# Optimization experiments

Measured on AMD Instinct MI355X. Metric: run time of the kernel, lower is better.

## Reference

```python
import jax, jax.numpy as jnp
import numpy as np

B, M, SV, OV, R, L, V, E = 256, 10, 32, 32, 128, 12, 1000, 64
M2 = M * M
STATE_DIM = (SV + 1) * M2  # 3300
OBJ_DIM = OV * M2          # 3200


def setup_inputs() -> dict:
    key = jax.random.key(0)
    ks = jax.random.split(key, 24)
    s = 0.02
    inp = {
        "state": jax.random.randint(ks[0], (B, M2), 0, SV),
        "obj": jax.random.randint(ks[1], (B, M2), 0, OV),
        "text": jax.random.randint(ks[2], (B, L), 0, V),
        # state MLP [STATE_DIM,128,128,R]
        "Ws1": jax.random.normal(ks[3], (STATE_DIM, 128)) * s,
        "bs1": jnp.zeros((128,)),
        "Ws2": jax.random.normal(ks[4], (128, 128)) * s,
        "bs2": jnp.zeros((128,)),
        "Ws3": jax.random.normal(ks[5], (128, R)) * s,
        "bs3": jnp.zeros((R,)),
        # object MLP [OBJ_DIM,128,128,R]
        "Wo1": jax.random.normal(ks[6], (OBJ_DIM, 128)) * s,
        "bo1": jnp.zeros((128,)),
        "Wo2": jax.random.normal(ks[7], (128, 128)) * s,
        "bo2": jnp.zeros((128,)),
        "Wo3": jax.random.normal(ks[8], (128, R)) * s,
        "bo3": jnp.zeros((R,)),
        # LSTM text encoder: embedding + single-layer LSTM with hidden=R
        "emb": jax.random.normal(ks[9], (V, E)) * s,
        "Wih": jax.random.normal(ks[10], (E, 4 * R)) * s,
        "Whh": jax.random.normal(ks[11], (R, 4 * R)) * s,
        "b_lstm": jnp.zeros((4 * R,)),
    }
    return inp


def _mlp(x, W1, b1, W2, b2, W3, b3):
    h = jax.nn.relu(x @ W1 + b1)
    h = jax.nn.relu(h @ W2 + b2)
    return h @ W3 + b3


def _lstm_last_hidden(text, emb, Wih, Whh, b):
    # text: (B, L) ids -> final hidden (B, R)
    x = emb[text]                      # (B, L, E)
    xs = jnp.swapaxes(x, 0, 1)         # (L, B, E)
    h0 = jnp.zeros((text.shape[0], R), x.dtype)
    c0 = jnp.zeros((text.shape[0], R), x.dtype)

    def step(carry, xt):
        h, c = carry
        g = xt @ Wih + h @ Whh + b     # (B, 4R)
        i, f, gg, o = jnp.split(g, 4, axis=-1)
        c = jax.nn.sigmoid(f) * c + jax.nn.sigmoid(i) * jnp.tanh(gg)
        h = jax.nn.sigmoid(o) * jnp.tanh(c)
        return (h, c), None

    (h, _), _ = jax.lax.scan(step, (h0, c0), xs)
    return h


def reference(state, obj, text, Ws1, bs1, Ws2, bs2, Ws3, bs3,
              Wo1, bo1, Wo2, bo2, Wo3, bo3, emb, Wih, Whh, b_lstm):
    b = state.shape[0]
    # one-hot encodings (torch scatter_ over channel dim)
    state_oh = jax.nn.one_hot(state, SV, dtype=jnp.float32)   # (B, 100, SV)
    obj_oh = jax.nn.one_hot(obj, OV, dtype=jnp.float32)       # (B, 100, OV)

    # repeat each map map_dim^2 times; copy p gets a one-hot of agent position p
    pos = jnp.eye(M2, dtype=jnp.float32)[None, :, :, None]    # (1, 100 copies, 100 cells, 1)
    state_rep = jnp.broadcast_to(state_oh[:, None], (b, M2, M2, SV))
    state_inp = jnp.concatenate(
        [state_rep, jnp.broadcast_to(pos, (b, M2, M2, 1))], axis=-1
    ).reshape(b * M2, STATE_DIM)
    obj_inp = jnp.broadcast_to(obj_oh[:, None], (b, M2, M2, OV)).reshape(b * M2, OBJ_DIM)

    state_out = _mlp(state_inp, Ws1, bs1, Ws2, bs2, Ws3, bs3)   # (B*100, R)
    object_out = _mlp(obj_inp, Wo1, bo1, Wo2, bo2, Wo3, bo3)    # (B*100, R)

    # text is identical across the 100 copies -> encode once, broadcast
    h = _lstm_last_hidden(text, emb, Wih, Whh, b_lstm)          # (B, R)
    lstm_out = jnp.broadcast_to(h[:, None], (b, M2, R)).reshape(b * M2, R)

    values = state_out * object_out * lstm_out                 # (B*100, R)
    map_pred = values.sum(1).reshape(b, M, M)
    return map_pred
```

## Files before the change

kernel.cpp:

```cpp
#include <hip/hip_runtime.h>


#define B_   256
#define M2_  100
#define R_   128
#define L_   12
#define E_   64
#define NT   1024

typedef _Float16 half2v __attribute__((ext_vector_type(2)));
typedef _Float16 f16x8  __attribute__((ext_vector_type(8)));
typedef float    f32x4  __attribute__((ext_vector_type(4)));

__device__ __forceinline__ float sigf(float x) { return 1.f / (1.f + expf(-x)); }

__device__ __forceinline__ uint pk16(float a, float b) {
    half2v h; h.x = (_Float16)a; h.y = (_Float16)b;
    return __builtin_bit_cast(uint, h);
}

__global__ __launch_bounds__(256) void pack_kernel(
    const float* __restrict__ Whh, const float* __restrict__ Wih,
    const float* __restrict__ Ws2, void* __restrict__ wsv)
{
    _Float16* WhhT = (_Float16*)wsv;
    _Float16* WihT = WhhT + 65536;
    uint*     W2P  = (uint*)(WihT + 32768);
    int g = blockIdx.x * 256 + threadIdx.x;
    if (g < 65536) {
        int r = g >> 9, c = g & 511;
        WhhT[c * 128 + r] = (_Float16)Whh[r * 512 + c];
    } else if (g < 65536 + 32768) {
        int g2 = g - 65536;
        int e = g2 >> 9, c = g2 & 511;
        WihT[c * 64 + e] = (_Float16)Wih[e * 512 + c];
    } else if (g < 65536 + 32768 + 8192) {
        int g3 = g - 65536 - 32768;
        int jp = g3 >> 7, kk = g3 & 127;
        W2P[g3] = pk16(Ws2[(2 * jp) * R_ + kk], Ws2[(2 * jp + 1) * R_ + kk]);
    }
}

__global__ __launch_bounds__(NT) __attribute__((amdgpu_waves_per_eu(4, 4)))
void uvfa_kernel(
    const int* __restrict__ state, const int* __restrict__ obj, const int* __restrict__ text,
    const float* __restrict__ Ws1, const float* __restrict__ bs1,
    const float* __restrict__ bs2, const float* __restrict__ Ws3, const float* __restrict__ bs3,
    const float* __restrict__ Wo1, const float* __restrict__ bo1,
    const float* __restrict__ Wo2, const float* __restrict__ bo2,
    const float* __restrict__ Wo3, const float* __restrict__ bo3,
    const float* __restrict__ emb, const float* __restrict__ b_lstm,
    const _Float16* __restrict__ WhhT, const _Float16* __restrict__ WihT,
    const uint* __restrict__ W2P,
    float* __restrict__ out)
{
    const int b   = blockIdx.x;
    const int tid = threadIdx.x;

    __shared__ __align__(16) uint  U[16064];
    __shared__ __align__(16) float part[NT];
    __shared__ __align__(16) float hbuf[R_];
    __shared__ __align__(16) uint  hpair[R_ / 2];
    __shared__ __align__(16) float tmp[R_], tmp2[R_], wbuf[R_], ubuf[R_], bsbuf[R_];
    __shared__ float redw2[2][112];
    __shared__ int   idx_o[M2_], idx_s[M2_], tids[L_];
    __shared__ float c0s;

    float* xw   = (float*)U;
    float* xemb = (float*)(U + 8192);

    const int lane = tid & 63;
    const int wv   = tid >> 6;
    const int m16  = lane & 15;
    const int kgrp = lane >> 4;

    f16x8 af[2][4];
    #pragma unroll
    for (int tt = 0; tt < 2; ++tt) {
        int col = (2 * wv + tt) * 16 + m16;
        #pragma unroll
        for (int s = 0; s < 4; ++s)
            af[tt][s] = *(const f16x8*)&WhhT[col * 128 + s * 32 + kgrp * 8];
    }

    if (tid < M2_) idx_o[tid] = obj[b * M2_ + tid];
    else if (tid >= 128 && tid < 128 + M2_) idx_s[tid - 128] = state[b * M2_ + tid - 128];
    else if (tid >= 256 && tid < 256 + L_) tids[tid - 256] = text[b * L_ + tid - 256];
    else if (tid >= 384 && tid < 448) hpair[tid - 384] = 0u;
    __syncthreads();
    if (tid < L_ * E_) xemb[(tid >> 6) * 66 + (tid & 63)] = emb[tids[tid >> 6] * E_ + (tid & 63)];
    else if (tid < L_ * E_ + 264) ((float*)(U + 8192 + 792))[tid - L_ * E_] = 0.f;
    __syncthreads();

    {
        f16x8 ax[2];
        #pragma unroll
        for (int s = 0; s < 2; ++s) {
            #pragma unroll
            for (int e = 0; e < 8; ++e)
                ax[s][e] = (_Float16)xemb[m16 * 66 + s * 32 + kgrp * 8 + e];
        }
        #pragma unroll
        for (int h = 0; h < 2; ++h) {
            int col = (wv * 2 + h) * 16 + m16;
            float bl = b_lstm[col];
            f32x4 acc = { bl, bl, bl, bl };
            #pragma unroll
            for (int s = 0; s < 2; ++s) {
                f16x8 bx = *(const f16x8*)&WihT[col * 64 + s * 32 + kgrp * 8];
                acc = __builtin_amdgcn_mfma_f32_16x16x32_f16(ax[s], bx, acc, 0, 0, 0);
            }
            if (kgrp < 3) {
                #pragma unroll
                for (int r = 0; r < 4; ++r)
                    xw[(kgrp * 4 + r) * 512 + col] = acc[r];
            }
        }
    }
    __syncthreads();

    float cst = 0.f;
    for (int t = 0; t < L_; ++t) {
        f16x8 bf[4];
        #pragma unroll
        for (int s = 0; s < 4; ++s) {
            uint4 hb = *(const uint4*)&hpair[s * 16 + kgrp * 4];
            bf[s] = __builtin_bit_cast(f16x8, hb);
        }
        #pragma unroll
        for (int tt = 0; tt < 2; ++tt) {
            int colb = (2 * wv + tt) * 16 + kgrp * 4;
            f32x4 acc = *(const f32x4*)&xw[t * 512 + colb];
            #pragma unroll
            for (int s = 0; s < 4; ++s)
                acc = __builtin_amdgcn_mfma_f32_16x16x32_f16(af[tt][s], bf[s], acc, 0, 0, 0);
            if (m16 == 0) {
                part[colb + 0] = acc[0];
                part[colb + 1] = acc[1];
                part[colb + 2] = acc[2];
                part[colb + 3] = acc[3];
            }
        }
        __syncthreads();
        if (tid < R_) {
            float gi = part[tid], gf = part[R_ + tid], gg = part[2 * R_ + tid], go = part[3 * R_ + tid];
            cst = sigf(gf) * cst + sigf(gi) * tanhf(gg);
            float hn = sigf(go) * tanhf(cst);
            hbuf[tid] = hn;
            float hs = __shfl_down(hn, 1, 64);
            if (!(tid & 1)) hpair[tid >> 1] = pk16(hn, hs);
        }
        __syncthreads();
    }

    {
        const uint4* src = (const uint4*)W2P;
        #pragma unroll
        for (int idx = tid; idx < 2048; idx += NT) {
            uint4 v = src[idx];
            int jp = idx >> 5, kq = idx & 31;
            *(uint4*)&U[jp * 132 + kq * 4] = v;
        }
    }

    const int k = tid & 127, qq = tid >> 7;
    {
        float acc = 0.f;
        int c0i = qq * 13, c1i = c0i + 13 < M2_ ? c0i + 13 : M2_;
        for (int c = c0i; c < c1i; ++c)
            acc += Wo1[(c * 32 + idx_o[c]) * R_ + k];
        part[qq * R_ + k] = acc;
    }
    __syncthreads();
    if (tid < R_) {
        float a = bo1[tid];
        #pragma unroll
        for (int q8 = 0; q8 < 8; ++q8) a += part[q8 * R_ + tid];
        tmp[tid] = fmaxf(a, 0.f);
    }
    __syncthreads();
    {
        float s0 = 0.f, s1 = 0.f, s2 = 0.f, s3 = 0.f;
        int j0 = qq * 16;
        #pragma unroll
        for (int j = 0; j < 16; j += 4) {
            s0 = fmaf(tmp[j0 + j + 0], Wo2[(j0 + j + 0) * R_ + k], s0);
            s1 = fmaf(tmp[j0 + j + 1], Wo2[(j0 + j + 1) * R_ + k], s1);
            s2 = fmaf(tmp[j0 + j + 2], Wo2[(j0 + j + 2) * R_ + k], s2);
            s3 = fmaf(tmp[j0 + j + 3], Wo2[(j0 + j + 3) * R_ + k], s3);
        }
        part[qq * R_ + k] = (s0 + s1) + (s2 + s3);
    }
    __syncthreads();
    if (tid < R_) {
        float a = bo2[tid];
        #pragma unroll
        for (int q8 = 0; q8 < 8; ++q8) a += part[q8 * R_ + tid];
        tmp2[tid] = fmaxf(a, 0.f);
    }
    __syncthreads();
    {
        float s0 = 0.f, s1 = 0.f, s2 = 0.f, s3 = 0.f;
        int j0 = qq * 16;
        #pragma unroll
        for (int j = 0; j < 16; j += 4) {
            s0 = fmaf(tmp2[j0 + j + 0], Wo3[(j0 + j + 0) * R_ + k], s0);
            s1 = fmaf(tmp2[j0 + j + 1], Wo3[(j0 + j + 1) * R_ + k], s1);
            s2 = fmaf(tmp2[j0 + j + 2], Wo3[(j0 + j + 2) * R_ + k], s2);
            s3 = fmaf(tmp2[j0 + j + 3], Wo3[(j0 + j + 3) * R_ + k], s3);
        }
        part[qq * R_ + k] = (s0 + s1) + (s2 + s3);
    }
    __syncthreads();
    if (tid < R_) {
        float a = bo3[tid];
        #pragma unroll
        for (int q8 = 0; q8 < 8; ++q8) a += part[q8 * R_ + tid];
        wbuf[tid] = a * hbuf[tid];
    }
    __syncthreads();

    {
        float s0 = 0.f, s1 = 0.f, s2 = 0.f, s3 = 0.f;
        int j0 = qq * 16;
        const float4* w3 = reinterpret_cast<const float4*>(&Ws3[k * R_ + j0]);
        #pragma unroll
        for (int jj = 0; jj < 4; ++jj) {
            float4 v = w3[jj];
            s0 = fmaf(v.x, wbuf[j0 + jj * 4 + 0], s0);
            s1 = fmaf(v.y, wbuf[j0 + jj * 4 + 1], s1);
            s2 = fmaf(v.z, wbuf[j0 + jj * 4 + 2], s2);
            s3 = fmaf(v.w, wbuf[j0 + jj * 4 + 3], s3);
        }
        part[qq * R_ + k] = (s0 + s1) + (s2 + s3);
    }
    if (tid >= 960) {
        int j = tid - 960;
        float s = bs3[j] * wbuf[j] + bs3[j + 64] * wbuf[j + 64];
        s += __shfl_down(s, 32, 64);
        s += __shfl_down(s, 16, 64);
        s += __shfl_down(s, 8, 64);
        s += __shfl_down(s, 4, 64);
        s += __shfl_down(s, 2, 64);
        s += __shfl_down(s, 1, 64);
        if (j == 0) c0s = s;
    }
    __syncthreads();
    if (tid < R_) {
        float a = 0.f;
        #pragma unroll
        for (int q8 = 0; q8 < 8; ++q8) a += part[q8 * R_ + tid];
        ubuf[tid] = a;
    }
    __syncthreads();

    {
        float acc = 0.f;
        int c0i = qq * 13, c1i = c0i + 13 < M2_ ? c0i + 13 : M2_;
        for (int c = c0i; c < c1i; ++c)
            acc += Ws1[(c * 33 + idx_s[c]) * R_ + k];
        part[qq * R_ + k] = acc;
    }
    __syncthreads();
    if (tid < R_) {
        float a = bs1[tid];
        #pragma unroll
        for (int q8 = 0; q8 < 8; ++q8) a += part[q8 * R_ + tid];
        bsbuf[tid] = a;
    }
    __syncthreads();

    #pragma unroll 4
    for (int pass = 0; pass < 13; ++pass) {
        int idx = pass * NT + tid;
        if (idx < M2_ * R_) {
            int j = idx & 127, p = idx >> 7;
            float v = fmaxf(bsbuf[j] + Ws1[(p * 33 + 32) * R_ + j], 0.f);
            float v2 = __shfl_down(v, 1, 64);
            if (!(j & 1)) U[8448 + p * 68 + (j >> 1)] = pk16(v, v2);
        }
    }
    if (tid < 816) U[8448 + 6800 + tid] = 0u;
    __syncthreads();

    if (wv < 14) {
        const int mtile = wv >> 1, nhalf = wv & 1;
        const uint* Ap = U + 8448 + (mtile * 16 + m16) * 68;
        f16x8 A[4];
        #pragma unroll
        for (int s = 0; s < 4; ++s)
            A[s] = __builtin_bit_cast(f16x8, *(const uint4*)&Ap[s * 16 + kgrp * 4]);
        f32x4 acc[4] = { {0,0,0,0}, {0,0,0,0}, {0,0,0,0}, {0,0,0,0} };
        #pragma unroll
        for (int nt = 0; nt < 4; ++nt) {
            int ko = (nhalf * 4 + nt) * 16 + m16;
            #pragma unroll
            for (int s = 0; s < 4; ++s) {
                const uint* Bp = U + (s * 16 + kgrp * 4) * 132 + ko;
                uint4 bv = { Bp[0], Bp[132], Bp[264], Bp[396] };
                acc[nt] = __builtin_amdgcn_mfma_f32_16x16x32_f16(
                    A[s], __builtin_bit_cast(f16x8, bv), acc[nt], 0, 0, 0);
            }
        }
        float vs0 = 0.f, vs1 = 0.f, vs2 = 0.f, vs3 = 0.f;
        #pragma unroll
        for (int nt = 0; nt < 4; ++nt) {
            int ko = (nhalf * 4 + nt) * 16 + m16;
            float bb = bs2[ko], uu = ubuf[ko];
            vs0 = fmaf(fmaxf(acc[nt][0] + bb, 0.f), uu, vs0);
            vs1 = fmaf(fmaxf(acc[nt][1] + bb, 0.f), uu, vs1);
            vs2 = fmaf(fmaxf(acc[nt][2] + bb, 0.f), uu, vs2);
            vs3 = fmaf(fmaxf(acc[nt][3] + bb, 0.f), uu, vs3);
        }
        vs0 += __shfl_xor(vs0, 1, 64); vs0 += __shfl_xor(vs0, 2, 64);
        vs0 += __shfl_xor(vs0, 4, 64); vs0 += __shfl_xor(vs0, 8, 64);
        vs1 += __shfl_xor(vs1, 1, 64); vs1 += __shfl_xor(vs1, 2, 64);
        vs1 += __shfl_xor(vs1, 4, 64); vs1 += __shfl_xor(vs1, 8, 64);
        vs2 += __shfl_xor(vs2, 1, 64); vs2 += __shfl_xor(vs2, 2, 64);
        vs2 += __shfl_xor(vs2, 4, 64); vs2 += __shfl_xor(vs2, 8, 64);
        vs3 += __shfl_xor(vs3, 1, 64); vs3 += __shfl_xor(vs3, 2, 64);
        vs3 += __shfl_xor(vs3, 4, 64); vs3 += __shfl_xor(vs3, 8, 64);
        if (m16 == 0) {
            int pr = mtile * 16 + kgrp * 4;
            redw2[nhalf][pr + 0] = vs0;
            redw2[nhalf][pr + 1] = vs1;
            redw2[nhalf][pr + 2] = vs2;
            redw2[nhalf][pr + 3] = vs3;
        }
    }
    __syncthreads();

    if (tid < M2_)
        out[b * M2_ + tid] = c0s + redw2[0][tid] + redw2[1][tid];
}

extern "C" void kernel_launch(void* const* d_in, const int* in_sizes, int n_in,
                              void* d_out, int out_size, void* d_ws, size_t ws_size,
                              hipStream_t stream) {
    const int*   state  = (const int*)d_in[0];
    const int*   obj    = (const int*)d_in[1];
    const int*   text   = (const int*)d_in[2];
    const float* Ws1    = (const float*)d_in[3];
    const float* bs1    = (const float*)d_in[4];
    const float* Ws2    = (const float*)d_in[5];
    const float* bs2    = (const float*)d_in[6];
    const float* Ws3    = (const float*)d_in[7];
    const float* bs3    = (const float*)d_in[8];
    const float* Wo1    = (const float*)d_in[9];
    const float* bo1    = (const float*)d_in[10];
    const float* Wo2    = (const float*)d_in[11];
    const float* bo2    = (const float*)d_in[12];
    const float* Wo3    = (const float*)d_in[13];
    const float* bo3    = (const float*)d_in[14];
    const float* emb    = (const float*)d_in[15];
    const float* Wih    = (const float*)d_in[16];
    const float* Whh    = (const float*)d_in[17];
    const float* b_lstm = (const float*)d_in[18];
    float* out = (float*)d_out;

    _Float16* WhhT = (_Float16*)d_ws;
    _Float16* WihT = WhhT + 65536;
    uint*     W2P  = (uint*)(WihT + 32768);

    hipLaunchKernelGGL(pack_kernel, dim3(416), dim3(256), 0, stream, Whh, Wih, Ws2, d_ws);
    hipLaunchKernelGGL(uvfa_kernel, dim3(B_), dim3(NT), 0, stream,
                       state, obj, text, Ws1, bs1, bs2, Ws3, bs3,
                       Wo1, bo1, Wo2, bo2, Wo3, bo3, emb, b_lstm,
                       WhhT, WihT, W2P, out);
}
```

Before: 39.85 us.

## Split each batch across two 512-thread blocks with staggered phase ordering

The grid now has two blocks of 512 threads per batch element instead of one 1024-thread block. Each block recomputes the LSTM and the object and state first-layer work, then handles half of the 100 output positions in the final MFMA stage. The two blocks run the LSTM and MLP phases in opposite order, so their latency-bound serial sections can overlap on the device. The sigmoid and tanh now use fast __expf, and the Whh fragments are pinned in registers. In exchange, the shared preamble work is done twice, and the fast transcendentals lose some accuracy.

Result: slower. 46.52 us (+16.7%).

```diff
diff --git a/kernel.cpp b/kernel.cpp
--- a/kernel.cpp
+++ b/kernel.cpp
@@ -6,18 +6,21 @@
 #define R_   128
 #define L_   12
 #define E_   64
-#define NT   1024
+#define NT   512
 
 typedef _Float16 half2v __attribute__((ext_vector_type(2)));
 typedef _Float16 f16x8  __attribute__((ext_vector_type(8)));
 typedef float    f32x4  __attribute__((ext_vector_type(4)));
 
-__device__ __forceinline__ float sigf(float x) { return 1.f / (1.f + expf(-x)); }
+__device__ __forceinline__ float sigf(float x)   { return 1.f / (1.f + __expf(-x)); }
+__device__ __forceinline__ float tanhff(float x) { float e = __expf(-2.f * x); return (1.f - e) / (1.f + e); }
 
 __device__ __forceinline__ uint pk16(float a, float b) {
     half2v h; h.x = (_Float16)a; h.y = (_Float16)b;
     return __builtin_bit_cast(uint, h);
 }
+
+#define PINU4(v) asm volatile("" : "+v"(v.x), "+v"(v.y), "+v"(v.z), "+v"(v.w));
 
 __global__ __launch_bounds__(256) void pack_kernel(
     const float* __restrict__ Whh, const float* __restrict__ Wih,
@@ -29,14 +32,12 @@
     int g = blockIdx.x * 256 + threadIdx.x;
     if (g < 65536) {
         int r = g >> 9, c = g & 511;
-        WhhT[c * 128 + r] = (_Float16)Whh[r * 512 + c];
-    } else if (g < 65536 + 32768) {
-        int g2 = g - 65536;
-        int e = g2 >> 9, c = g2 & 511;
-        WihT[c * 64 + e] = (_Float16)Wih[e * 512 + c];
-    } else if (g < 65536 + 32768 + 8192) {
-        int g3 = g - 65536 - 32768;
-        int jp = g3 >> 7, kk = g3 & 127;
+        WhhT[c * 128 + r] = (_Float16)Whh[g];
+    } else if (g < 98304) {
+        int g2 = g - 65536; int e = g2 >> 9, c = g2 & 511;
+        WihT[c * 64 + e] = (_Float16)Wih[g2];
+    } else if (g < 106496) {
+        int g3 = g - 98304; int jp = g3 >> 7, kk = g3 & 127;
         W2P[g3] = pk16(Ws2[(2 * jp) * R_ + kk], Ws2[(2 * jp + 1) * R_ + kk]);
     }
 }
@@ -54,14 +55,15 @@
     const uint* __restrict__ W2P,
     float* __restrict__ out)
 {
-    const int b   = blockIdx.x;
-    const int tid = threadIdx.x;
+    const int b      = blockIdx.x & 255;
+    const int parity = blockIdx.x >> 8;
+    const int tid    = threadIdx.x;
 
     __shared__ __align__(16) uint  U[16064];
     __shared__ __align__(16) float part[NT];
     __shared__ __align__(16) float hbuf[R_];
     __shared__ __align__(16) uint  hpair[R_ / 2];
-    __shared__ __align__(16) float tmp[R_], tmp2[R_], wbuf[R_], ubuf[R_], bsbuf[R_];
+    __shared__ __align__(16) float tmp[R_], tmp2[R_], o3buf[R_], wbuf[R_], ubuf[R_], bsbuf[R_];
     __shared__ float redw2[2][112];
     __shared__ int   idx_o[M2_], idx_s[M2_], tids[L_];
     __shared__ float c0s;
@@ -73,169 +75,200 @@
     const int wv   = tid >> 6;
     const int m16  = lane & 15;
     const int kgrp = lane >> 4;
-
-    f16x8 af[2][4];
-    #pragma unroll
-    for (int tt = 0; tt < 2; ++tt) {
-        int col = (2 * wv + tt) * 16 + m16;
-        #pragma unroll
-        for (int s = 0; s < 4; ++s)
-            af[tt][s] = *(const f16x8*)&WhhT[col * 128 + s * 32 + kgrp * 8];
-    }
+    const int k = tid & 127, qq = tid >> 7;
 
     if (tid < M2_) idx_o[tid] = obj[b * M2_ + tid];
     else if (tid >= 128 && tid < 128 + M2_) idx_s[tid - 128] = state[b * M2_ + tid - 128];
     else if (tid >= 256 && tid < 256 + L_) tids[tid - 256] = text[b * L_ + tid - 256];
     else if (tid >= 384 && tid < 448) hpair[tid - 384] = 0u;
     __syncthreads();
-    if (tid < L_ * E_) xemb[(tid >> 6) * 66 + (tid & 63)] = emb[tids[tid >> 6] * E_ + (tid & 63)];
-    else if (tid < L_ * E_ + 264) ((float*)(U + 8192 + 792))[tid - L_ * E_] = 0.f;
-    __syncthreads();
-
-    {
-        f16x8 ax[2];
+
+    auto do_lstm = [&]() {
+        for (int i = tid; i < L_ * E_; i += NT)
+            xemb[(i >> 6) * 66 + (i & 63)] = emb[tids[i >> 6] * E_ + (i & 63)];
+        if (tid < 264) ((float*)(U + 8192 + 792))[tid] = 0.f;
+        __syncthreads();
+        {
+            f16x8 ax[2];
+            #pragma unroll
+            for (int s = 0; s < 2; ++s)
+                #pragma unroll
+                for (int e = 0; e < 8; ++e)
+                    ax[s][e] = (_Float16)xemb[m16 * 66 + s * 32 + kgrp * 8 + e];
+            #pragma unroll
+            for (int h = 0; h < 4; ++h) {
+                int col = (wv * 4 + h) * 16 + m16;
+                float bl = b_lstm[col];
+                f32x4 acc = { bl, bl, bl, bl };
+                #pragma unroll
+                for (int s = 0; s < 2; ++s) {
+                    f16x8 bx = *(const f16x8*)&WihT[col * 64 + s * 32 + kgrp * 8];
+                    acc = __builtin_amdgcn_mfma_f32_16x16x32_f16(ax[s], bx, acc, 0, 0, 0);
+                }
+                if (kgrp < 3) {
+                    #pragma unroll
+                    for (int r = 0; r < 4; ++r)
+                        xw[(kgrp * 4 + r) * 512 + col] = acc[r];
+                }
+            }
+        }
+        uint4 afu[4][4];
         #pragma unroll
-        for (int s = 0; s < 2; ++s) {
-            #pragma unroll
-            for (int e = 0; e < 8; ++e)
-                ax[s][e] = (_Float16)xemb[m16 * 66 + s * 32 + kgrp * 8 + e];
-        }
-        #pragma unroll
-        for (int h = 0; h < 2; ++h) {
-            int col = (wv * 2 + h) * 16 + m16;
-            float bl = b_lstm[col];
-            f32x4 acc = { bl, bl, bl, bl };
-            #pragma unroll
-            for (int s = 0; s < 2; ++s) {
-                f16x8 bx = *(const f16x8*)&WihT[col * 64 + s * 32 + kgrp * 8];
-                acc = __builtin_amdgcn_mfma_f32_16x16x32_f16(ax[s], bx, acc, 0, 0, 0);
-            }
-            if (kgrp < 3) {
+        for (int g = 0; g < 4; ++g) {
+            int col = (wv + 8 * g) * 16 + m16;
+            #pragma unroll
+            for (int s = 0; s < 4; ++s) {
+                afu[g][s] = *(const uint4*)&WhhT[col * 128 + s * 32 + kgrp * 8];
+                PINU4(afu[g][s])
+            }
+        }
+        __syncthreads();
+        float cst = 0.f;
+        for (int t = 0; t < L_; ++t) {
+            f16x8 bf[4];
+            #pragma unroll
+            for (int s = 0; s < 4; ++s)
+                bf[s] = __builtin_bit_cast(f16x8, *(const uint4*)&hpair[s * 16 + kgrp * 4]);
+            #pragma unroll
+            for (int g = 0; g < 4; ++g) {
+                int colb = (wv + 8 * g) * 16 + kgrp * 4;
+                f32x4 acc = *(const f32x4*)&xw[t * 512 + colb];
                 #pragma unroll
-                for (int r = 0; r < 4; ++r)
-                    xw[(kgrp * 4 + r) * 512 + col] = acc[r];
-            }
-        }
-    }
-    __syncthreads();
-
-    float cst = 0.f;
-    for (int t = 0; t < L_; ++t) {
-        f16x8 bf[4];
-        #pragma unroll
-        for (int s = 0; s < 4; ++s) {
-            uint4 hb = *(const uint4*)&hpair[s * 16 + kgrp * 4];
-            bf[s] = __builtin_bit_cast(f16x8, hb);
-        }
-        #pragma unroll
-        for (int tt = 0; tt < 2; ++tt) {
-            int colb = (2 * wv + tt) * 16 + kgrp * 4;
-            f32x4 acc = *(const f32x4*)&xw[t * 512 + colb];
-            #pragma unroll
-            for (int s = 0; s < 4; ++s)
-                acc = __builtin_amdgcn_mfma_f32_16x16x32_f16(af[tt][s], bf[s], acc, 0, 0, 0);
-            if (m16 == 0) {
-                part[colb + 0] = acc[0];
-                part[colb + 1] = acc[1];
-                part[colb + 2] = acc[2];
-                part[colb + 3] = acc[3];
-            }
-        }
-        __syncthreads();
-        if (tid < R_) {
-            float gi = part[tid], gf = part[R_ + tid], gg = part[2 * R_ + tid], go = part[3 * R_ + tid];
-            cst = sigf(gf) * cst + sigf(gi) * tanhf(gg);
-            float hn = sigf(go) * tanhf(cst);
-            hbuf[tid] = hn;
-            float hs = __shfl_down(hn, 1, 64);
-            if (!(tid & 1)) hpair[tid >> 1] = pk16(hn, hs);
-        }
-        __syncthreads();
-    }
-
-    {
-        const uint4* src = (const uint4*)W2P;
-        #pragma unroll
-        for (int idx = tid; idx < 2048; idx += NT) {
-            uint4 v = src[idx];
-            int jp = idx >> 5, kq = idx & 31;
-            *(uint4*)&U[jp * 132 + kq * 4] = v;
-        }
-    }
-
-    const int k = tid & 127, qq = tid >> 7;
-    {
-        float acc = 0.f;
-        int c0i = qq * 13, c1i = c0i + 13 < M2_ ? c0i + 13 : M2_;
-        for (int c = c0i; c < c1i; ++c)
-            acc += Wo1[(c * 32 + idx_o[c]) * R_ + k];
-        part[qq * R_ + k] = acc;
-    }
-    __syncthreads();
-    if (tid < R_) {
-        float a = bo1[tid];
-        #pragma unroll
-        for (int q8 = 0; q8 < 8; ++q8) a += part[q8 * R_ + tid];
-        tmp[tid] = fmaxf(a, 0.f);
-    }
+                for (int s = 0; s < 4; ++s)
+                    acc = __builtin_amdgcn_mfma_f32_16x16x32_f16(
+                        __builtin_bit_cast(f16x8, afu[g][s]), bf[s], acc, 0, 0, 0);
+                if (m16 == 0) {
+                    part[colb + 0] = acc[0];
+                    part[colb + 1] = acc[1];
+                    part[colb + 2] = acc[2];
+                    part[colb + 3] = acc[3];
+                }
+            }
+            __syncthreads();
+            if (tid < R_) {
+                float gi = part[tid], gf = part[R_ + tid], gg = part[2 * R_ + tid], go = part[3 * R_ + tid];
+                cst = sigf(gf) * cst + sigf(gi) * tanhff(gg);
+                float hn = sigf(go) * tanhff(cst);
+                hbuf[tid] = hn;
+                float hs = __shfl_down(hn, 1, 64);
+                if (!(tid & 1)) hpair[tid >> 1] = pk16(hn, hs);
+            }
+            __syncthreads();
+        }
+        {
+            const uint4* src = (const uint4*)W2P;
+            #pragma unroll
+            for (int idx = tid; idx < 2048; idx += NT) {
+                uint4 v = src[idx];
+                int jp = idx >> 5, kq = idx & 31;
+                *(uint4*)&U[jp * 132 + kq * 4] = v;
+            }
+        }
+    };
+
+    auto do_objmlp = [&]() {
+        {
+            float acc = 0.f;
+            #pragma unroll 5
+            for (int c = qq * 25; c < qq * 25 + 25; ++c)
+                acc += Wo1[(c * 32 + idx_o[c]) * R_ + k];
+            part[qq * R_ + k] = acc;
+        }
+        __syncthreads();
+        if (tid < R_)
+            tmp[tid] = fmaxf(bo1[tid] + part[tid] + part[R_ + tid] + part[2 * R_ + tid] + part[3 * R_ + tid], 0.f);
+        __syncthreads();
+        {
+            float s0 = 0.f, s1 = 0.f, s2 = 0.f, s3 = 0.f;
+            int j0 = qq * 32;
+            #pragma unroll
+            for (int j = 0; j < 32; j += 4) {
+                s0 = fmaf(tmp[j0 + j + 0], Wo2[(j0 + j + 0) * R_ + k], s0);
+                s1 = fmaf(tmp[j0 + j + 1], Wo2[(j0 + j + 1) * R_ + k], s1);
+                s2 = fmaf(tmp[j0 + j + 2], Wo2[(j0 + j + 2) * R_ + k], s2);
+                s3 = fmaf(tmp[j0 + j + 3], Wo2[(j0 + j + 3) * R_ + k], s3);
+            }
+            part[qq * R_ + k] = (s0 + s1) + (s2 + s3);
+        }
+        __syncthreads();
+        if (tid < R_)
+            tmp2[tid] = fmaxf(bo2[tid] + part[tid] + part[R_ + tid] + part[2 * R_ + tid] + part[3 * R_ + tid], 0.f);
+        __syncthreads();
+        {
+            float s0 = 0.f, s1 = 0.f, s2 = 0.f, s3 = 0.f;
+            int j0 = qq * 32;
+            #pragma unroll
+            for (int j = 0; j < 32; j += 4) {
+                s0 = fmaf(tmp2[j0 + j + 0], Wo3[(j0 + j + 0) * R_ + k], s0);
+                s1 = fmaf(tmp2[j0 + j + 1], Wo3[(j0 + j + 1) * R_ + k], s1);
+                s2 = fmaf(tmp2[j0 + j + 2], Wo3[(j0 + j + 2) * R_ + k], s2);
+                s3 = fmaf(tmp2[j0 + j + 3], Wo3[(j0 + j + 3) * R_ + k], s3);
+            }
+            part[qq * R_ + k] = (s0 + s1) + (s2 + s3);
+        }
+        __syncthreads();
+        if (tid < R_)
+            o3buf[tid] = bo3[tid] + part[tid] + part[R_ + tid] + part[2 * R_ + tid] + part[3 * R_ + tid];
+        __syncthreads();
+    };
+
+    auto do_bases = [&]() {
+        {
+            float acc = 0.f;
+            #pragma unroll 5
+            for (int c = qq * 25; c < qq * 25 + 25; ++c)
+                acc += Ws1[(c * 33 + idx_s[c]) * R_ + k];
+            part[qq * R_ + k] = acc;
+        }
+        __syncthreads();
+        if (tid < R_)
+            bsbuf[tid] = bs1[tid] + part[tid] + part[R_ + tid] + part[2 * R_ + tid] + part[3 * R_ + tid];
+        __syncthreads();
+    };
+
+    auto do_h1p = [&]() {
+        #pragma unroll 5
+        for (int pass = 0; pass < 25; ++pass) {
+            int idx = pass * NT + tid;
+            int j = idx & 127, p = idx >> 7;
+            float v = fmaxf(bsbuf[j] + Ws1[(p * 33 + 32) * R_ + j], 0.f);
+            float v2 = __shfl_down(v, 1, 64);
+            if (!(j & 1)) U[8448 + p * 68 + (j >> 1)] = pk16(v, v2);
+        }
+        for (int i = tid; i < 816; i += NT) U[8448 + 6800 + i] = 0u;
+    };
+
+    if (!parity) {
+        do_lstm();
+        do_objmlp();
+        do_bases();
+        do_h1p();
+    } else {
+        do_objmlp();
+        do_bases();
+        do_lstm();
+        do_h1p();
+    }
+    __syncthreads();
+
+    if (tid < R_) wbuf[tid] = o3buf[tid] * hbuf[tid];
     __syncthreads();
     {
         float s0 = 0.f, s1 = 0.f, s2 = 0.f, s3 = 0.f;
-        int j0 = qq * 16;
+        const float4* w4 = reinterpret_cast<const float4*>(&Ws3[k * R_ + qq * 32]);
         #pragma unroll
-        for (int j = 0; j < 16; j += 4) {
-            s0 = fmaf(tmp[j0 + j + 0], Wo2[(j0 + j + 0) * R_ + k], s0);
-            s1 = fmaf(tmp[j0 + j + 1], Wo2[(j0 + j + 1) * R_ + k], s1);
-            s2 = fmaf(tmp[j0 + j + 2], Wo2[(j0 + j + 2) * R_ + k], s2);
-            s3 = fmaf(tmp[j0 + j + 3], Wo2[(j0 + j + 3) * R_ + k], s3);
+        for (int jj = 0; jj < 8; ++jj) {
+            float4 v = w4[jj];
+            int j0 = qq * 32 + jj * 4;
+            s0 = fmaf(v.x, wbuf[j0 + 0], s0);
+            s1 = fmaf(v.y, wbuf[j0 + 1], s1);
+            s2 = fmaf(v.z, wbuf[j0 + 2], s2);
+            s3 = fmaf(v.w, wbuf[j0 + 3], s3);
         }
         part[qq * R_ + k] = (s0 + s1) + (s2 + s3);
     }
-    __syncthreads();
-    if (tid < R_) {
-        float a = bo2[tid];
-        #pragma unroll
-        for (int q8 = 0; q8 < 8; ++q8) a += part[q8 * R_ + tid];
-        tmp2[tid] = fmaxf(a, 0.f);
-    }
-    __syncthreads();
-    {
-        float s0 = 0.f, s1 = 0.f, s2 = 0.f, s3 = 0.f;
-        int j0 = qq * 16;
-        #pragma unroll
-        for (int j = 0; j < 16; j += 4) {
-            s0 = fmaf(tmp2[j0 + j + 0], Wo3[(j0 + j + 0) * R_ + k], s0);
-            s1 = fmaf(tmp2[j0 + j + 1], Wo3[(j0 + j + 1) * R_ + k], s1);
-            s2 = fmaf(tmp2[j0 + j + 2], Wo3[(j0 + j + 2) * R_ + k], s2);
-            s3 = fmaf(tmp2[j0 + j + 3], Wo3[(j0 + j + 3) * R_ + k], s3);
-        }
-        part[qq * R_ + k] = (s0 + s1) + (s2 + s3);
-    }
-    __syncthreads();
-    if (tid < R_) {
-        float a = bo3[tid];
-        #pragma unroll
-        for (int q8 = 0; q8 < 8; ++q8) a += part[q8 * R_ + tid];
-        wbuf[tid] = a * hbuf[tid];
-    }
-    __syncthreads();
-
-    {
-        float s0 = 0.f, s1 = 0.f, s2 = 0.f, s3 = 0.f;
-        int j0 = qq * 16;
-        const float4* w3 = reinterpret_cast<const float4*>(&Ws3[k * R_ + j0]);
-        #pragma unroll
-        for (int jj = 0; jj < 4; ++jj) {
-            float4 v = w3[jj];
-            s0 = fmaf(v.x, wbuf[j0 + jj * 4 + 0], s0);
-            s1 = fmaf(v.y, wbuf[j0 + jj * 4 + 1], s1);
-            s2 = fmaf(v.z, wbuf[j0 + jj * 4 + 2], s2);
-            s3 = fmaf(v.w, wbuf[j0 + jj * 4 + 3], s3);
-        }
-        part[qq * R_ + k] = (s0 + s1) + (s2 + s3);
-    }
-    if (tid >= 960) {
-        int j = tid - 960;
+    if (tid >= 448) {
+        int j = tid - 448;
         float s = bs3[j] * wbuf[j] + bs3[j + 64] * wbuf[j + 64];
         s += __shfl_down(s, 32, 64);
         s += __shfl_down(s, 16, 64);
@@ -246,92 +279,67 @@
         if (j == 0) c0s = s;
     }
     __syncthreads();
-    if (tid < R_) {
-        float a = 0.f;
-        #pragma unroll
-        for (int q8 = 0; q8 < 8; ++q8) a += part[q8 * R_ + tid];
-        ubuf[tid] = a;
-    }
+    if (tid < R_)
+        ubuf[tid] = part[tid] + part[R_ + tid] + part[2 * R_ + tid] + part[3 * R_ + tid];
     __syncthreads();
 
     {
-        float acc = 0.f;
-        int c0i = qq * 13, c1i = c0i + 13 < M2_ ? c0i + 13 : M2_;
-        for (int c = c0i; c < c1i; ++c)
-            acc += Ws1[(c * 33 + idx_s[c]) * R_ + k];
-        part[qq * R_ + k] = acc;
-    }
-    __syncthreads();
-    if (tid < R_) {
-        float a = bs1[tid];
-        #pragma unroll
-        for (int q8 = 0; q8 < 8; ++q8) a += part[q8 * R_ + tid];
-        bsbuf[tid] = a;
-    }
-    __syncthreads();
-
-    #pragma unroll 4
-    for (int pass = 0; pass < 13; ++pass) {
-        int idx = pass * NT + tid;
-        if (idx < M2_ * R_) {
-            int j = idx & 127, p = idx >> 7;
-            float v = fmaxf(bsbuf[j] + Ws1[(p * 33 + 32) * R_ + j], 0.f);
-            float v2 = __shfl_down(v, 1, 64);
-            if (!(j & 1)) U[8448 + p * 68 + (j >> 1)] = pk16(v, v2);
-        }
-    }
-    if (tid < 816) U[8448 + 6800 + tid] = 0u;
-    __syncthreads();
-
-    if (wv < 14) {
-        const int mtile = wv >> 1, nhalf = wv & 1;
-        const uint* Ap = U + 8448 + (mtile * 16 + m16) * 68;
-        f16x8 A[4];
-        #pragma unroll
-        for (int s = 0; s < 4; ++s)
-            A[s] = __builtin_bit_cast(f16x8, *(const uint4*)&Ap[s * 16 + kgrp * 4]);
-        f32x4 acc[4] = { {0,0,0,0}, {0,0,0,0}, {0,0,0,0}, {0,0,0,0} };
-        #pragma unroll
-        for (int nt = 0; nt < 4; ++nt) {
-            int ko = (nhalf * 4 + nt) * 16 + m16;
-            #pragma unroll
-            for (int s = 0; s < 4; ++s) {
-                const uint* Bp = U + (s * 16 + kgrp * 4) * 132 + ko;
-                uint4 bv = { Bp[0], Bp[132], Bp[264], Bp[396] };
-                acc[nt] = __builtin_amdgcn_mfma_f32_16x16x32_f16(
-                    A[s], __builtin_bit_cast(f16x8, bv), acc[nt], 0, 0, 0);
-            }
-        }
-        float vs0 = 0.f, vs1 = 0.f, vs2 = 0.f, vs3 = 0.f;
-        #pragma unroll
-        for (int nt = 0; nt < 4; ++nt) {
-            int ko = (nhalf * 4 + nt) * 16 + m16;
-            float bb = bs2[ko], uu = ubuf[ko];
-            vs0 = fmaf(fmaxf(acc[nt][0] + bb, 0.f), uu, vs0);
-            vs1 = fmaf(fmaxf(acc[nt][1] + bb, 0.f), uu, vs1);
-            vs2 = fmaf(fmaxf(acc[nt][2] + bb, 0.f), uu, vs2);
-            vs3 = fmaf(fmaxf(acc[nt][3] + bb, 0.f), uu, vs3);
-        }
-        vs0 += __shfl_xor(vs0, 1, 64); vs0 += __shfl_xor(vs0, 2, 64);
-        vs0 += __shfl_xor(vs0, 4, 64); vs0 += __shfl_xor(vs0, 8, 64);
-        vs1 += __shfl_xor(vs1, 1, 64); vs1 += __shfl_xor(vs1, 2, 64);
-        vs1 += __shfl_xor(vs1, 4, 64); vs1 += __shfl_xor(vs1, 8, 64);
-        vs2 += __shfl_xor(vs2, 1, 64); vs2 += __shfl_xor(vs2, 2, 64);
-        vs2 += __shfl_xor(vs2, 4, 64); vs2 += __shfl_xor(vs2, 8, 64);
-        vs3 += __shfl_xor(vs3, 1, 64); vs3 += __shfl_xor(vs3, 2, 64);
-        vs3 += __shfl_xor(vs3, 4, 64); vs3 += __shfl_xor(vs3, 8, 64);
-        if (m16 == 0) {
-            int pr = mtile * 16 + kgrp * 4;
-            redw2[nhalf][pr + 0] = vs0;
-            redw2[nhalf][pr + 1] = vs1;
-            redw2[nhalf][pr + 2] = vs2;
-            redw2[nhalf][pr + 3] = vs3;
-        }
-    }
-    __syncthreads();
-
-    if (tid < M2_)
-        out[b * M2_ + tid] = c0s + redw2[0][tid] + redw2[1][tid];
+        const int nmt = parity ? 3 : 4;
+        const int mt0 = parity ? 4 : 0;
+        if (wv < 2 * nmt) {
+            const int mtile = mt0 + (wv >> 1), nhalf = wv & 1;
+            const uint* Ap = U + 8448 + (mtile * 16 + m16) * 68;
+            f16x8 A[4];
+            #pragma unroll
+            for (int s = 0; s < 4; ++s)
+                A[s] = __builtin_bit_cast(f16x8, *(const uint4*)&Ap[s * 16 + kgrp * 4]);
+            f32x4 acc[4] = { {0,0,0,0}, {0,0,0,0}, {0,0,0,0}, {0,0,0,0} };
+            #pragma unroll
+            for (int nt = 0; nt < 4; ++nt) {
+                int ko = (nhalf * 4 + nt) * 16 + m16;
+                #pragma unroll
+                for (int s = 0; s < 4; ++s) {
+                    const uint* Bp = U + (s * 16 + kgrp * 4) * 132 + ko;
+                    uint4 bv = { Bp[0], Bp[132], Bp[264], Bp[396] };
+                    acc[nt] = __builtin_amdgcn_mfma_f32_16x16x32_f16(
+                        A[s], __builtin_bit_cast(f16x8, bv), acc[nt], 0, 0, 0);
+                }
+            }
+            float vs0 = 0.f, vs1 = 0.f, vs2 = 0.f, vs3 = 0.f;
+            #pragma unroll
+            for (int nt = 0; nt < 4; ++nt) {
+                int ko = (nhalf * 4 + nt) * 16 + m16;
+                float bb = bs2[ko], uu = ubuf[ko];
+                vs0 = fmaf(fmaxf(acc[nt][0] + bb, 0.f), uu, vs0);
+                vs1 = fmaf(fmaxf(acc[nt][1] + bb, 0.f), uu, vs1);
+                vs2 = fmaf(fmaxf(acc[nt][2] + bb, 0.f), uu, vs2);
+                vs3 = fmaf(fmaxf(acc[nt][3] + bb, 0.f), uu, vs3);
+            }
+            vs0 += __shfl_xor(vs0, 1, 64); vs0 += __shfl_xor(vs0, 2, 64);
+            vs0 += __shfl_xor(vs0, 4, 64); vs0 += __shfl_xor(vs0, 8, 64);
+            vs1 += __shfl_xor(vs1, 1, 64); vs1 += __shfl_xor(vs1, 2, 64);
+            vs1 += __shfl_xor(vs1, 4, 64); vs1 += __shfl_xor(vs1, 8, 64);
+            vs2 += __shfl_xor(vs2, 1, 64); vs2 += __shfl_xor(vs2, 2, 64);
+            vs2 += __shfl_xor(vs2, 4, 64); vs2 += __shfl_xor(vs2, 8, 64);
+            vs3 += __shfl_xor(vs3, 1, 64); vs3 += __shfl_xor(vs3, 2, 64);
+            vs3 += __shfl_xor(vs3, 4, 64); vs3 += __shfl_xor(vs3, 8, 64);
+            if (m16 == 0) {
+                int pr = mtile * 16 + kgrp * 4;
+                redw2[nhalf][pr + 0] = vs0;
+                redw2[nhalf][pr + 1] = vs1;
+                redw2[nhalf][pr + 2] = vs2;
+                redw2[nhalf][pr + 3] = vs3;
+            }
+        }
+    }
+    __syncthreads();
+
+    {
+        const int p0 = parity ? 64 : 0;
+        const int p1 = parity ? M2_ : 64;
+        if (tid >= p0 && tid < p1)
+            out[b * M2_ + tid] = c0s + redw2[0][tid] + redw2[1][tid];
+    }
 }
 
 extern "C" void kernel_launch(void* const* d_in, const int* in_sizes, int n_in,
@@ -363,7 +371,7 @@
     uint*     W2P  = (uint*)(WihT + 32768);
 
     hipLaunchKernelGGL(pack_kernel, dim3(416), dim3(256), 0, stream, Whh, Wih, Ws2, d_ws);
-    hipLaunchKernelGGL(uvfa_kernel, dim3(B_), dim3(NT), 0, stream,
+    hipLaunchKernelGGL(uvfa_kernel, dim3(512), dim3(NT), 0, stream,
                        state, obj, text, Ws1, bs1, bs2, Ws3, bs3,
                        Wo1, bo1, Wo2, bo2, Wo3, bo3, emb, b_lstm,
                        WhhT, WihT, W2P, out);
```

## Warp-specialize LSTM recurrence and overlap embedding-sum gathers with it

Applied to the files above, without the earlier changes.

Splits the 16 waves into two groups. Eight waves run the LSTM recurrence with each lane holding four gate tiles, so the gate nonlinearities are computed in registers and one barrier per step is removed. The other eight waves do the Wo1 and Ws1 row gathers and the W2 staging during the recurrence steps, so that global-load latency overlaps the serial LSTM chain. Also switches to fast __expf-based sigmoid and tanh, double-buffers the packed h vector, and coalesces reads in the pack kernel. This costs more registers for the pinned Whh fragments, more LDS, and some accuracy from the fast exp.

After: 44.86 us. 12.6% more time.

```diff
diff --git a/kernel.cpp b/kernel.cpp
--- a/kernel.cpp
+++ b/kernel.cpp
@@ -12,12 +12,15 @@
 typedef _Float16 f16x8  __attribute__((ext_vector_type(8)));
 typedef float    f32x4  __attribute__((ext_vector_type(4)));
 
-__device__ __forceinline__ float sigf(float x) { return 1.f / (1.f + expf(-x)); }
+__device__ __forceinline__ float sigf(float x)   { return 1.f / (1.f + __expf(-x)); }
+__device__ __forceinline__ float tanhff(float x) { float e = __expf(-2.f * x); return (1.f - e) / (1.f + e); }
 
 __device__ __forceinline__ uint pk16(float a, float b) {
     half2v h; h.x = (_Float16)a; h.y = (_Float16)b;
     return __builtin_bit_cast(uint, h);
 }
+
+#define PINU4(v) asm volatile("" : "+v"(v.x), "+v"(v.y), "+v"(v.z), "+v"(v.w));
 
 __global__ __launch_bounds__(256) void pack_kernel(
     const float* __restrict__ Whh, const float* __restrict__ Wih,
@@ -29,14 +32,12 @@
     int g = blockIdx.x * 256 + threadIdx.x;
     if (g < 65536) {
         int r = g >> 9, c = g & 511;
-        WhhT[c * 128 + r] = (_Float16)Whh[r * 512 + c];
-    } else if (g < 65536 + 32768) {
-        int g2 = g - 65536;
-        int e = g2 >> 9, c = g2 & 511;
-        WihT[c * 64 + e] = (_Float16)Wih[e * 512 + c];
-    } else if (g < 65536 + 32768 + 8192) {
-        int g3 = g - 65536 - 32768;
-        int jp = g3 >> 7, kk = g3 & 127;
+        WhhT[c * 128 + r] = (_Float16)Whh[g];
+    } else if (g < 98304) {
+        int g2 = g - 65536; int e = g2 >> 9, c = g2 & 511;
+        WihT[c * 64 + e] = (_Float16)Wih[g2];
+    } else if (g < 106496) {
+        int g3 = g - 98304; int jp = g3 >> 7, kk = g3 & 127;
         W2P[g3] = pk16(Ws2[(2 * jp) * R_ + kk], Ws2[(2 * jp + 1) * R_ + kk]);
     }
 }
@@ -57,52 +58,60 @@
     const int b   = blockIdx.x;
     const int tid = threadIdx.x;
 
-    __shared__ __align__(16) uint  U[16064];
+    __shared__ __align__(16) uint  U[22208];
     __shared__ __align__(16) float part[NT];
     __shared__ __align__(16) float hbuf[R_];
-    __shared__ __align__(16) uint  hpair[R_ / 2];
+    __shared__ __align__(16) uint  hpair[2][64];
     __shared__ __align__(16) float tmp[R_], tmp2[R_], wbuf[R_], ubuf[R_], bsbuf[R_];
     __shared__ float redw2[2][112];
     __shared__ int   idx_o[M2_], idx_s[M2_], tids[L_];
     __shared__ float c0s;
 
     float* xw   = (float*)U;
-    float* xemb = (float*)(U + 8192);
+    float* xemb = (float*)(U + 14592);
 
     const int lane = tid & 63;
     const int wv   = tid >> 6;
     const int m16  = lane & 15;
     const int kgrp = lane >> 4;
-
-    f16x8 af[2][4];
-    #pragma unroll
-    for (int tt = 0; tt < 2; ++tt) {
-        int col = (2 * wv + tt) * 16 + m16;
-        #pragma unroll
-        for (int s = 0; s < 4; ++s)
-            af[tt][s] = *(const f16x8*)&WhhT[col * 128 + s * 32 + kgrp * 8];
-    }
+    const int k    = tid & 127;
+    const int qq   = tid >> 7;
+    const int tid2 = tid - 512;
+    const int q2u  = (tid >> 7) & 3;
 
     if (tid < M2_) idx_o[tid] = obj[b * M2_ + tid];
     else if (tid >= 128 && tid < 128 + M2_) idx_s[tid - 128] = state[b * M2_ + tid - 128];
     else if (tid >= 256 && tid < 256 + L_) tids[tid - 256] = text[b * L_ + tid - 256];
-    else if (tid >= 384 && tid < 448) hpair[tid - 384] = 0u;
-    __syncthreads();
-    if (tid < L_ * E_) xemb[(tid >> 6) * 66 + (tid & 63)] = emb[tids[tid >> 6] * E_ + (tid & 63)];
-    else if (tid < L_ * E_ + 264) ((float*)(U + 8192 + 792))[tid - L_ * E_] = 0.f;
-    __syncthreads();
-
-    {
+    else if (tid >= 384 && tid < 448) hpair[0][tid - 384] = 0u;
+    __syncthreads();
+
+    if (wv < 8) {
+        for (int i = tid; i < 16 * 66; i += 512) {
+            int t = i / 66, c = i - t * 66;
+            xemb[i] = (c < 64 && t < L_) ? emb[tids[t] * E_ + c] : 0.f;
+        }
+    } else {
+        const uint4* src = (const uint4*)W2P;
+        #pragma unroll
+        for (int idx = tid2; idx < 2048; idx += 512) {
+            uint4 v = src[idx];
+            int jp = idx >> 5, kq = idx & 31;
+            *(uint4*)&U[6144 + jp * 132 + kq * 4] = v;
+        }
+    }
+    __syncthreads();
+
+    float accO = 0.f, accS = 0.f;
+    if (wv < 8) {
         f16x8 ax[2];
         #pragma unroll
-        for (int s = 0; s < 2; ++s) {
+        for (int s = 0; s < 2; ++s)
             #pragma unroll
             for (int e = 0; e < 8; ++e)
                 ax[s][e] = (_Float16)xemb[m16 * 66 + s * 32 + kgrp * 8 + e];
-        }
-        #pragma unroll
-        for (int h = 0; h < 2; ++h) {
-            int col = (wv * 2 + h) * 16 + m16;
+        #pragma unroll
+        for (int h = 0; h < 4; ++h) {
+            int col = (wv * 4 + h) * 16 + m16;
             float bl = b_lstm[col];
             f32x4 acc = { bl, bl, bl, bl };
             #pragma unroll
@@ -116,69 +125,99 @@
                     xw[(kgrp * 4 + r) * 512 + col] = acc[r];
             }
         }
-    }
-    __syncthreads();
-
-    float cst = 0.f;
+    } else {
+        int c0r = q2u * 25;
+        #pragma unroll
+        for (int c = 0; c < 5; ++c)
+            accO += Wo1[((c0r + c) * 32 + idx_o[c0r + c]) * R_ + k];
+    }
+
+    uint4 afu[4][4];
+    if (wv < 8) {
+        #pragma unroll
+        for (int g = 0; g < 4; ++g) {
+            int col = (wv + 8 * g) * 16 + m16;
+            #pragma unroll
+            for (int s = 0; s < 4; ++s) {
+                afu[g][s] = *(const uint4*)&WhhT[col * 128 + s * 32 + kgrp * 8];
+                PINU4(afu[g][s])
+            }
+        }
+    }
+    __syncthreads();
+
+    float cst0 = 0.f, cst1 = 0.f, cst2 = 0.f, cst3 = 0.f;
+    float h0 = 0.f, h1v = 0.f, h2v = 0.f, h3v = 0.f;
     for (int t = 0; t < L_; ++t) {
-        f16x8 bf[4];
-        #pragma unroll
-        for (int s = 0; s < 4; ++s) {
-            uint4 hb = *(const uint4*)&hpair[s * 16 + kgrp * 4];
-            bf[s] = __builtin_bit_cast(f16x8, hb);
-        }
-        #pragma unroll
-        for (int tt = 0; tt < 2; ++tt) {
-            int colb = (2 * wv + tt) * 16 + kgrp * 4;
-            f32x4 acc = *(const f32x4*)&xw[t * 512 + colb];
+        if (wv < 8) {
+            const uint* hp = hpair[t & 1];
+            f16x8 bf[4];
             #pragma unroll
             for (int s = 0; s < 4; ++s)
-                acc = __builtin_amdgcn_mfma_f32_16x16x32_f16(af[tt][s], bf[s], acc, 0, 0, 0);
+                bf[s] = __builtin_bit_cast(f16x8, *(const uint4*)&hp[s * 16 + kgrp * 4]);
+            f32x4 acc[4];
+            #pragma unroll
+            for (int g = 0; g < 4; ++g) {
+                acc[g] = *(const f32x4*)&xw[t * 512 + (wv + 8 * g) * 16 + kgrp * 4];
+                #pragma unroll
+                for (int s = 0; s < 4; ++s)
+                    acc[g] = __builtin_amdgcn_mfma_f32_16x16x32_f16(
+                        __builtin_bit_cast(f16x8, afu[g][s]), bf[s], acc[g], 0, 0, 0);
+            }
+            cst0 = sigf(acc[1][0]) * cst0 + sigf(acc[0][0]) * tanhff(acc[2][0]);
+            h0   = sigf(acc[3][0]) * tanhff(cst0);
+            cst1 = sigf(acc[1][1]) * cst1 + sigf(acc[0][1]) * tanhff(acc[2][1]);
+            h1v  = sigf(acc[3][1]) * tanhff(cst1);
+            cst2 = sigf(acc[1][2]) * cst2 + sigf(acc[0][2]) * tanhff(acc[2][2]);
+            h2v  = sigf(acc[3][2]) * tanhff(cst2);
+            cst3 = sigf(acc[1][3]) * cst3 + sigf(acc[0][3]) * tanhff(acc[2][3]);
+            h3v  = sigf(acc[3][3]) * tanhff(cst3);
             if (m16 == 0) {
-                part[colb + 0] = acc[0];
-                part[colb + 1] = acc[1];
-                part[colb + 2] = acc[2];
-                part[colb + 3] = acc[3];
+                uint* hw = hpair[(t + 1) & 1];
+                hw[8 * wv + kgrp * 2]     = pk16(h0, h1v);
+                hw[8 * wv + kgrp * 2 + 1] = pk16(h2v, h3v);
+            }
+        } else {
+            int c0r = q2u * 25;
+            if (t < 4) {
+                #pragma unroll
+                for (int c = 0; c < 5; ++c) {
+                    int cr = c0r + 5 + 5 * t + c;
+                    accO += Wo1[(cr * 32 + idx_o[cr]) * R_ + k];
+                }
+            } else if (t == 4) {
+                part[tid2] = accO;
+            } else if (t == 5) {
+                if (tid2 < R_)
+                    tmp[tid2] = fmaxf(bo1[tid2] + part[tid2] + part[128 + tid2] + part[256 + tid2] + part[384 + tid2], 0.f);
+                #pragma unroll
+                for (int c = 0; c < 5; ++c)
+                    accS += Ws1[((c0r + c) * 33 + idx_s[c0r + c]) * R_ + k];
+            } else if (t < 10) {
+                #pragma unroll
+                for (int c = 0; c < 5; ++c) {
+                    int cr = c0r + 5 + 5 * (t - 6) + c;
+                    accS += Ws1[(cr * 33 + idx_s[cr]) * R_ + k];
+                }
+            } else if (t == 10) {
+                part[tid2] = accS;
+            } else {
+                if (tid2 < R_)
+                    bsbuf[tid2] = bs1[tid2] + part[tid2] + part[128 + tid2] + part[256 + tid2] + part[384 + tid2];
             }
         }
         __syncthreads();
-        if (tid < R_) {
-            float gi = part[tid], gf = part[R_ + tid], gg = part[2 * R_ + tid], go = part[3 * R_ + tid];
-            cst = sigf(gf) * cst + sigf(gi) * tanhf(gg);
-            float hn = sigf(go) * tanhf(cst);
-            hbuf[tid] = hn;
-            float hs = __shfl_down(hn, 1, 64);
-            if (!(tid & 1)) hpair[tid >> 1] = pk16(hn, hs);
-        }
-        __syncthreads();
-    }
-
-    {
-        const uint4* src = (const uint4*)W2P;
-        #pragma unroll
-        for (int idx = tid; idx < 2048; idx += NT) {
-            uint4 v = src[idx];
-            int jp = idx >> 5, kq = idx & 31;
-            *(uint4*)&U[jp * 132 + kq * 4] = v;
-        }
-    }
-
-    const int k = tid & 127, qq = tid >> 7;
-    {
-        float acc = 0.f;
-        int c0i = qq * 13, c1i = c0i + 13 < M2_ ? c0i + 13 : M2_;
-        for (int c = c0i; c < c1i; ++c)
-            acc += Wo1[(c * 32 + idx_o[c]) * R_ + k];
-        part[qq * R_ + k] = acc;
-    }
-    __syncthreads();
-    if (tid < R_) {
-        float a = bo1[tid];
-        #pragma unroll
-        for (int q8 = 0; q8 < 8; ++q8) a += part[q8 * R_ + tid];
-        tmp[tid] = fmaxf(a, 0.f);
-    }
-    __syncthreads();
+    }
+
+    if (wv < 8 && m16 == 0) {
+        int j = wv * 16 + kgrp * 4;
+        hbuf[j + 0] = h0;
+        hbuf[j + 1] = h1v;
+        hbuf[j + 2] = h2v;
+        hbuf[j + 3] = h3v;
+    }
+    __syncthreads();
+
     {
         float s0 = 0.f, s1 = 0.f, s2 = 0.f, s3 = 0.f;
         int j0 = qq * 16;
@@ -245,31 +284,6 @@
         s += __shfl_down(s, 1, 64);
         if (j == 0) c0s = s;
     }
-    __syncthreads();
-    if (tid < R_) {
-        float a = 0.f;
-        #pragma unroll
-        for (int q8 = 0; q8 < 8; ++q8) a += part[q8 * R_ + tid];
-        ubuf[tid] = a;
-    }
-    __syncthreads();
-
-    {
-        float acc = 0.f;
-        int c0i = qq * 13, c1i = c0i + 13 < M2_ ? c0i + 13 : M2_;
-        for (int c = c0i; c < c1i; ++c)
-            acc += Ws1[(c * 33 + idx_s[c]) * R_ + k];
-        part[qq * R_ + k] = acc;
-    }
-    __syncthreads();
-    if (tid < R_) {
-        float a = bs1[tid];
-        #pragma unroll
-        for (int q8 = 0; q8 < 8; ++q8) a += part[q8 * R_ + tid];
-        bsbuf[tid] = a;
-    }
-    __syncthreads();
-
     #pragma unroll 4
     for (int pass = 0; pass < 13; ++pass) {
         int idx = pass * NT + tid;
@@ -277,15 +291,22 @@
             int j = idx & 127, p = idx >> 7;
             float v = fmaxf(bsbuf[j] + Ws1[(p * 33 + 32) * R_ + j], 0.f);
             float v2 = __shfl_down(v, 1, 64);
-            if (!(j & 1)) U[8448 + p * 68 + (j >> 1)] = pk16(v, v2);
-        }
-    }
-    if (tid < 816) U[8448 + 6800 + tid] = 0u;
+            if (!(j & 1)) U[14592 + p * 68 + (j >> 1)] = pk16(v, v2);
+        }
+    }
+    if (tid < 816) U[14592 + 6800 + tid] = 0u;
+    __syncthreads();
+    if (tid < R_) {
+        float a = 0.f;
+        #pragma unroll
+        for (int q8 = 0; q8 < 8; ++q8) a += part[q8 * R_ + tid];
+        ubuf[tid] = a;
+    }
     __syncthreads();
 
     if (wv < 14) {
         const int mtile = wv >> 1, nhalf = wv & 1;
-        const uint* Ap = U + 8448 + (mtile * 16 + m16) * 68;
+        const uint* Ap = U + 14592 + (mtile * 16 + m16) * 68;
         f16x8 A[4];
         #pragma unroll
         for (int s = 0; s < 4; ++s)
@@ -296,7 +317,7 @@
             int ko = (nhalf * 4 + nt) * 16 + m16;
             #pragma unroll
             for (int s = 0; s < 4; ++s) {
-                const uint* Bp = U + (s * 16 + kgrp * 4) * 132 + ko;
+                const uint* Bp = U + 6144 + (s * 16 + kgrp * 4) * 132 + ko;
                 uint4 bv = { Bp[0], Bp[132], Bp[264], Bp[396] };
                 acc[nt] = __builtin_amdgcn_mfma_f32_16x16x32_f16(
                     A[s], __builtin_bit_cast(f16x8, bv), acc[nt], 0, 0, 0);
```
